# Performance work log

Hardware: AMD Instinct MI355X
Metric: run time of the kernel (lower is better)

Reference implementation:

```python
import jax, jax.numpy as jnp
import numpy as np


def _bilinear_ac(img, H, W):
    """Bilinear resize with align_corners=True. img: [B, C, h, w] -> [B, C, H, W]."""
    B, C, h, w = img.shape
    ys = jnp.linspace(0.0, h - 1.0, H)
    xs = jnp.linspace(0.0, w - 1.0, W)
    y0 = jnp.floor(ys).astype(jnp.int32)
    x0 = jnp.floor(xs).astype(jnp.int32)
    y1 = jnp.minimum(y0 + 1, h - 1)
    x1 = jnp.minimum(x0 + 1, w - 1)
    wy = (ys - y0).astype(img.dtype)  # [H]
    wx = (xs - x0).astype(img.dtype)  # [W]
    top = img[:, :, y0, :]            # [B, C, H, w]
    bot = img[:, :, y1, :]
    row = top * (1.0 - wy)[None, None, :, None] + bot * wy[None, None, :, None]
    left = row[:, :, :, x0]           # [B, C, H, W]
    right = row[:, :, :, x1]
    return left * (1.0 - wx)[None, None, None, :] + right * wx[None, None, None, :]


def setup_inputs() -> dict:
    key = jax.random.key(0)
    k1, k2, k3 = jax.random.split(key, 3)
    B, F, h, w = 16, 256, 64, 64
    H, W = 512, 512
    K = 21
    feature_map = jax.random.normal(k1, (B, F, h, w), dtype=jnp.float32)
    x = jax.random.uniform(k2, (B, 3, H, W), dtype=jnp.float32)
    conv_w = jax.random.normal(k3, (K, F), dtype=jnp.float32) * 0.05
    conv_b = jnp.zeros((K,), dtype=jnp.float32)
    return {"feature_map": feature_map, "x": x, "conv_w": conv_w, "conv_b": conv_b}


def reference(feature_map, x, conv_w, conv_b):
    B, _, H, W = x.shape
    # 1x1 conv: feature_dim -> num_classes
    logits = jnp.einsum('bfhw,kf->bkhw', feature_map, conv_w) + conv_b[None, :, None, None]
    seg = jax.nn.softmax(logits, axis=1)                 # [B, K, h, w]
    seg = _bilinear_ac(seg, H, W)                        # [B, K, H, W]
    xp = jnp.transpose(x, (0, 2, 3, 1))                  # [B, H, W, C]
    # per-class masked mean pooling (the python loop, fused into one einsum)
    q = jnp.einsum('bhwc,bkhw->bkc', xp, seg) / (H * W)  # [B, K, C]
    # broadcast dot-product attention maps
    attn = jnp.einsum('bhwc,bkc->bkhw', xp, q)           # [B, K, H, W]
    return attn
```

## Files before the change

kernel.cpp:

```cpp
#include <hip/hip_runtime.h>

#define BN 16
#define FD 256
#define SH 64
#define SW 64
#define BH 512
#define BW 512
#define KN 21
#define SP (SH*SW)
#define BP (BH*BW)

__device__ __forceinline__ float adj_w(int big, int small) {
    double t = (double)big * (63.0 / 511.0);
    int i0 = (int)t;
    double fr = t - (double)i0;
    int i1 = i0 + 1; if (i1 > 63) i1 = 63;
    float w = 0.0f;
    if (i0 == small) w += (float)(1.0 - fr);
    if (i1 == small) w += (float)fr;
    return w;
}

__device__ __forceinline__ void adj_range(int small, int& lo, int& hi) {
    lo = (int)floorf((small - 1) * (511.0f / 63.0f)); if (lo < 0) lo = 0;
    hi = (int)ceilf((small + 1) * (511.0f / 63.0f));  if (hi > 511) hi = 511;
}

__global__ __launch_bounds__(256) void k_seg(const float* __restrict__ fm,
                                             const float* __restrict__ cw,
                                             const float* __restrict__ cb,
                                             float* __restrict__ seg) {
    int gid = blockIdx.x * 256 + threadIdx.x;
    int b = gid >> 12;
    int p = gid & (SP - 1);
    const float* fmb = fm + (size_t)b * FD * SP + p;

    float acc[KN];
#pragma unroll
    for (int k = 0; k < KN; ++k) acc[k] = 0.0f;

#pragma unroll 4
    for (int f = 0; f < FD; ++f) {
        float v = fmb[(size_t)f * SP];
#pragma unroll
        for (int k = 0; k < KN; ++k)
            acc[k] = fmaf(v, cw[k * FD + f], acc[k]);
    }

    float mx = -1e30f;
#pragma unroll
    for (int k = 0; k < KN; ++k) { acc[k] += cb[k]; mx = fmaxf(mx, acc[k]); }
    float s = 0.0f;
#pragma unroll
    for (int k = 0; k < KN; ++k) { acc[k] = expf(acc[k] - mx); s += acc[k]; }
    float inv = 1.0f / s;

    float* segb = seg + (size_t)b * KN * SP + p;
#pragma unroll
    for (int k = 0; k < KN; ++k) segb[(size_t)k * SP] = acc[k] * inv;
}

__global__ __launch_bounds__(256) void k_downx(const float* __restrict__ x,
                                               float* __restrict__ tmpA) {
    int gid = blockIdx.x * 256 + threadIdx.x;
    int s  = gid & 63;
    int Y  = (gid >> 6) & 511;
    int bc = gid >> 15;
    const float* row = x + ((size_t)bc * BH + Y) * BW;
    int lo, hi; adj_range(s, lo, hi);
    float acc = 0.0f;
    for (int X = lo; X <= hi; ++X) acc = fmaf(adj_w(X, s), row[X], acc);
    tmpA[gid] = acc;
}

__global__ __launch_bounds__(256) void k_downy(const float* __restrict__ tmpA,
                                               float* __restrict__ xd) {
    int gid = blockIdx.x * 256 + threadIdx.x;
    int s  = gid & 63;
    int r  = (gid >> 6) & 63;
    int bc = gid >> 12;
    const float* base = tmpA + (size_t)bc * BH * SW + s;
    int lo, hi; adj_range(r, lo, hi);
    float acc = 0.0f;
    for (int Y = lo; Y <= hi; ++Y) acc = fmaf(adj_w(Y, r), base[(size_t)Y * SW], acc);
    xd[gid] = acc;
}

__global__ __launch_bounds__(256) void k_q(const float* __restrict__ seg,
                                           const float* __restrict__ xd,
                                           float* __restrict__ q) {
    int b = blockIdx.x / KN, k = blockIdx.x % KN;
    const float* sg = seg + ((size_t)b * KN + k) * SP;
    const float* xb = xd + (size_t)b * 3 * SP;
    float a0 = 0.f, a1 = 0.f, a2 = 0.f;
    for (int p = threadIdx.x; p < SP; p += 256) {
        float sv = sg[p];
        a0 = fmaf(sv, xb[p], a0);
        a1 = fmaf(sv, xb[SP + p], a1);
        a2 = fmaf(sv, xb[2 * SP + p], a2);
    }
    __shared__ float red[3][256];
    red[0][threadIdx.x] = a0; red[1][threadIdx.x] = a1; red[2][threadIdx.x] = a2;
    __syncthreads();
    for (int off = 128; off > 0; off >>= 1) {
        if (threadIdx.x < (unsigned)off) {
            red[0][threadIdx.x] += red[0][threadIdx.x + off];
            red[1][threadIdx.x] += red[1][threadIdx.x + off];
            red[2][threadIdx.x] += red[2][threadIdx.x + off];
        }
        __syncthreads();
    }
    if (threadIdx.x == 0) {
        const float scale = 1.0f / (float)BP;
        float* qo = q + ((size_t)b * KN + k) * 3;
        qo[0] = red[0][0] * scale;
        qo[1] = red[1][0] * scale;
        qo[2] = red[2][0] * scale;
    }
}

__global__ __launch_bounds__(256) void k_attn(const float* __restrict__ x,
                                              const float* __restrict__ q,
                                              float* __restrict__ out) {
    __shared__ float qs[KN * 3];
    int b   = blockIdx.x >> 8;
    int blk = blockIdx.x & 255;
    if (threadIdx.x < KN * 3) qs[threadIdx.x] = q[(size_t)b * KN * 3 + threadIdx.x];
    __syncthreads();

    int p4 = blk * 256 + threadIdx.x;
    const float4* xb = (const float4*)(x + (size_t)b * 3 * BP);
    float4 x0 = xb[p4];
    float4 x1 = xb[BP / 4 + p4];
    float4 x2 = xb[2 * (BP / 4) + p4];
    float4* ob = (float4*)(out + (size_t)b * KN * BP) + p4;
#pragma unroll
    for (int k = 0; k < KN; ++k) {
        float q0 = qs[k * 3], q1 = qs[k * 3 + 1], q2 = qs[k * 3 + 2];
        float4 r;
        r.x = fmaf(x0.x, q0, fmaf(x1.x, q1, x2.x * q2));
        r.y = fmaf(x0.y, q0, fmaf(x1.y, q1, x2.y * q2));
        r.z = fmaf(x0.z, q0, fmaf(x1.z, q1, x2.z * q2));
        r.w = fmaf(x0.w, q0, fmaf(x1.w, q1, x2.w * q2));
        ob[(size_t)k * (BP / 4)] = r;
    }
}

extern "C" void kernel_launch(void* const* d_in, const int* in_sizes, int n_in,
                              void* d_out, int out_size, void* d_ws, size_t ws_size,
                              hipStream_t stream) {
    const float* fm = (const float*)d_in[0];
    const float* x  = (const float*)d_in[1];
    const float* cw = (const float*)d_in[2];
    const float* cb = (const float*)d_in[3];
    float* out = (float*)d_out;

    float* seg  = (float*)d_ws;
    float* tmpA = seg  + (size_t)BN * KN * SP;
    float* xd   = tmpA + (size_t)BN * 3 * BH * SW;
    float* q    = xd   + (size_t)BN * 3 * SP;

    k_seg  <<<BN * SP / 256,            256, 0, stream>>>(fm, cw, cb, seg);
    k_downx<<<BN * 3 * BH * SW / 256,   256, 0, stream>>>(x, tmpA);
    k_downy<<<BN * 3 * SP / 256,        256, 0, stream>>>(tmpA, xd);
    k_q    <<<BN * KN,                  256, 0, stream>>>(seg, xd, q);
    k_attn <<<BN * (BP / 1024),         256, 0, stream>>>(x, q, out);
}
```

Measured before the change: 539.5 us.

## Merge seg and downx launches, vectorize seg over 4 pixels, nontemporal attn stores

Combines the 1x1-conv/softmax kernel and the horizontal downsample into one launch, split by block index. The seg part now handles four pixels per thread with vector loads and stores, so it needs only 64 blocks. In the attention kernel, the x loads are issued before the q barrier and outputs are written with nontemporal stores to cut cache pollution on the large write. The trade-off is that the 64 heavy seg blocks, each carrying 84 vector accumulator registers, may become a tail inside the fused launch.

```diff
diff --git a/kernel.cpp b/kernel.cpp
--- a/kernel.cpp
+++ b/kernel.cpp
@@ -9,6 +9,11 @@
 #define KN 21
 #define SP (SH*SW)
 #define BP (BH*BW)
+
+#define SEG_BLOCKS 64
+#define DOWNX_BLOCKS (BN*3*BH*SW/256)
+
+typedef float f32x4 __attribute__((ext_vector_type(4)));
 
 __device__ __forceinline__ float adj_w(int big, int small) {
     double t = (double)big * (63.0 / 511.0);
@@ -26,43 +31,54 @@
     hi = (int)ceilf((small + 1) * (511.0f / 63.0f));  if (hi > 511) hi = 511;
 }
 
-__global__ __launch_bounds__(256) void k_seg(const float* __restrict__ fm,
-                                             const float* __restrict__ cw,
-                                             const float* __restrict__ cb,
-                                             float* __restrict__ seg) {
-    int gid = blockIdx.x * 256 + threadIdx.x;
-    int b = gid >> 12;
-    int p = gid & (SP - 1);
-    const float* fmb = fm + (size_t)b * FD * SP + p;
+__device__ __forceinline__ void seg_body(int blk, int tid,
+                                         const float* __restrict__ fm,
+                                         const float* __restrict__ cw,
+                                         const float* __restrict__ cb,
+                                         float* __restrict__ seg) {
+    int gid = blk * 256 + tid;
+    int b   = gid >> 10;
+    int p4  = gid & 1023;
+    const f32x4* fmb = (const f32x4*)(fm + (size_t)b * FD * SP) + p4;
 
-    float acc[KN];
+    f32x4 acc[KN];
 #pragma unroll
-    for (int k = 0; k < KN; ++k) acc[k] = 0.0f;
+    for (int k = 0; k < KN; ++k) acc[k] = (f32x4)0.0f;
 
-#pragma unroll 4
+#pragma unroll 2
     for (int f = 0; f < FD; ++f) {
-        float v = fmb[(size_t)f * SP];
+        f32x4 v = fmb[f * (SP / 4)];
 #pragma unroll
         for (int k = 0; k < KN; ++k)
-            acc[k] = fmaf(v, cw[k * FD + f], acc[k]);
+            acc[k] += v * cw[k * FD + f];
     }
 
-    float mx = -1e30f;
+    f32x4 mx = (f32x4)(-1e30f);
 #pragma unroll
-    for (int k = 0; k < KN; ++k) { acc[k] += cb[k]; mx = fmaxf(mx, acc[k]); }
-    float s = 0.0f;
+    for (int k = 0; k < KN; ++k) {
+        acc[k] += cb[k];
+        mx.x = fmaxf(mx.x, acc[k].x); mx.y = fmaxf(mx.y, acc[k].y);
+        mx.z = fmaxf(mx.z, acc[k].z); mx.w = fmaxf(mx.w, acc[k].w);
+    }
+    f32x4 s = (f32x4)0.0f;
 #pragma unroll
-    for (int k = 0; k < KN; ++k) { acc[k] = expf(acc[k] - mx); s += acc[k]; }
-    float inv = 1.0f / s;
+    for (int k = 0; k < KN; ++k) {
+        acc[k].x = expf(acc[k].x - mx.x); acc[k].y = expf(acc[k].y - mx.y);
+        acc[k].z = expf(acc[k].z - mx.z); acc[k].w = expf(acc[k].w - mx.w);
+        s += acc[k];
+    }
+    f32x4 inv;
+    inv.x = 1.0f / s.x; inv.y = 1.0f / s.y; inv.z = 1.0f / s.z; inv.w = 1.0f / s.w;
 
-    float* segb = seg + (size_t)b * KN * SP + p;
+    f32x4* segb = (f32x4*)(seg + (size_t)b * KN * SP) + p4;
 #pragma unroll
-    for (int k = 0; k < KN; ++k) segb[(size_t)k * SP] = acc[k] * inv;
+    for (int k = 0; k < KN; ++k) segb[k * (SP / 4)] = acc[k] * inv;
 }
 
-__global__ __launch_bounds__(256) void k_downx(const float* __restrict__ x,
-                                               float* __restrict__ tmpA) {
-    int gid = blockIdx.x * 256 + threadIdx.x;
+__device__ __forceinline__ void downx_body(int blk, int tid,
+                                           const float* __restrict__ x,
+                                           float* __restrict__ tmpA) {
+    int gid = blk * 256 + tid;
     int s  = gid & 63;
     int Y  = (gid >> 6) & 511;
     int bc = gid >> 15;
@@ -71,6 +87,16 @@
     float acc = 0.0f;
     for (int X = lo; X <= hi; ++X) acc = fmaf(adj_w(X, s), row[X], acc);
     tmpA[gid] = acc;
+}
+
+__global__ __launch_bounds__(256) void k_phase1(const float* __restrict__ fm,
+                                                const float* __restrict__ cw,
+                                                const float* __restrict__ cb,
+                                                const float* __restrict__ x,
+                                                float* __restrict__ seg,
+                                                float* __restrict__ tmpA) {
+    if (blockIdx.x < SEG_BLOCKS) seg_body(blockIdx.x, threadIdx.x, fm, cw, cb, seg);
+    else                         downx_body(blockIdx.x - SEG_BLOCKS, threadIdx.x, x, tmpA);
 }
 
 __global__ __launch_bounds__(256) void k_downy(const float* __restrict__ tmpA,
@@ -122,27 +148,25 @@
 __global__ __launch_bounds__(256) void k_attn(const float* __restrict__ x,
                                               const float* __restrict__ q,
                                               float* __restrict__ out) {
-    __shared__ float qs[KN * 3];
     int b   = blockIdx.x >> 8;
     int blk = blockIdx.x & 255;
+    int p4  = blk * 256 + threadIdx.x;
+
+    const f32x4* xb = (const f32x4*)(x + (size_t)b * 3 * BP);
+    f32x4 x0 = xb[p4];
+    f32x4 x1 = xb[BP / 4 + p4];
+    f32x4 x2 = xb[2 * (BP / 4) + p4];
+
+    __shared__ float qs[KN * 3];
     if (threadIdx.x < KN * 3) qs[threadIdx.x] = q[(size_t)b * KN * 3 + threadIdx.x];
     __syncthreads();
 
-    int p4 = blk * 256 + threadIdx.x;
-    const float4* xb = (const float4*)(x + (size_t)b * 3 * BP);
-    float4 x0 = xb[p4];
-    float4 x1 = xb[BP / 4 + p4];
-    float4 x2 = xb[2 * (BP / 4) + p4];
-    float4* ob = (float4*)(out + (size_t)b * KN * BP) + p4;
+    f32x4* ob = (f32x4*)(out + (size_t)b * KN * BP) + p4;
 #pragma unroll
     for (int k = 0; k < KN; ++k) {
         float q0 = qs[k * 3], q1 = qs[k * 3 + 1], q2 = qs[k * 3 + 2];
-        float4 r;
-        r.x = fmaf(x0.x, q0, fmaf(x1.x, q1, x2.x * q2));
-        r.y = fmaf(x0.y, q0, fmaf(x1.y, q1, x2.y * q2));
-        r.z = fmaf(x0.z, q0, fmaf(x1.z, q1, x2.z * q2));
-        r.w = fmaf(x0.w, q0, fmaf(x1.w, q1, x2.w * q2));
-        ob[(size_t)k * (BP / 4)] = r;
+        f32x4 r = x0 * q0 + x1 * q1 + x2 * q2;
+        __builtin_nontemporal_store(r, ob + (size_t)k * (BP / 4));
     }
 }
 
@@ -160,9 +184,8 @@
     float* xd   = tmpA + (size_t)BN * 3 * BH * SW;
     float* q    = xd   + (size_t)BN * 3 * SP;
 
-    k_seg  <<<BN * SP / 256,            256, 0, stream>>>(fm, cw, cb, seg);
-    k_downx<<<BN * 3 * BH * SW / 256,   256, 0, stream>>>(x, tmpA);
-    k_downy<<<BN * 3 * SP / 256,        256, 0, stream>>>(tmpA, xd);
-    k_q    <<<BN * KN,                  256, 0, stream>>>(seg, xd, q);
-    k_attn <<<BN * (BP / 1024),         256, 0, stream>>>(x, q, out);
+    k_phase1<<<SEG_BLOCKS + DOWNX_BLOCKS, 256, 0, stream>>>(fm, cw, cb, x, seg, tmpA);
+    k_downy <<<BN * 3 * SP / 256,         256, 0, stream>>>(tmpA, xd);
+    k_q     <<<BN * KN,                   256, 0, stream>>>(seg, xd, q);
+    k_attn  <<<BN * (BP / 1024),          256, 0, stream>>>(x, q, out);
 }
```

New measurement: 510.9 us. 5.3% less time.
